# Optimization experiments

Hardware: AMD Instinct MI355X
Metric: run time of the kernel (lower is better)

The kernel has to match this reference:

```python
import jax, jax.numpy as jnp
import numpy as np
from jax import lax

B, DIM, H, W = 16, 256, 64, 64
NH, KD = 8, 16
NH_KD = NH * KD        # 128
DH = 2 * NH_KD         # 256 (attn_ratio=2)
SCALE = KD ** -0.5
PE_LEN = 16


def conv1x1(x, Wt, b):
    # x: [B,Cin,H,W], Wt: [Cout,Cin]
    return jnp.einsum('oi,bihw->bohw', Wt, x) + b[None, :, None, None]


def dwconv3x3(x, Wt, b):
    # depthwise 3x3, pad 1. Wt: [C,1,3,3]
    C = x.shape[1]
    y = lax.conv_general_dilated(x, Wt, window_strides=(1, 1),
                                 padding=((1, 1), (1, 1)),
                                 feature_group_count=C,
                                 dimension_numbers=('NCHW', 'OIHW', 'NCHW'))
    return y + b[None, :, None, None]


def relu6(x):
    return jnp.clip(x, 0.0, 6.0)


def h_sigmoid(x):
    return jnp.clip(x + 3.0, 0.0, 6.0) / 6.0


def interp_linear(pe, N):
    # F.interpolate(mode='linear', align_corners=False). pe: [1,C,S] -> [1,C,N]
    S = pe.shape[-1]
    src = (jnp.arange(N, dtype=jnp.float32) + 0.5) * (S / N) - 0.5
    src = jnp.clip(src, 0.0, S - 1.0)
    lo = jnp.floor(src).astype(jnp.int32)
    hi = jnp.minimum(lo + 1, S - 1)
    w = (src - lo.astype(jnp.float32))[None, None, :]
    return pe[..., lo] * (1.0 - w) + pe[..., hi] * w


def axial_attn(qm, km, vm, pe_q, pe_k, N):
    # qm,km: [B,NH_KD,N] squeezed q/k means; vm: [B,DH,N]
    qn = (qm + interp_linear(pe_q, N)).reshape(B, NH, KD, N).transpose(0, 1, 3, 2)  # [B,h,N,kd]
    kn = (km + interp_linear(pe_k, N)).reshape(B, NH, KD, N)                        # [B,h,kd,N]
    vn = vm.reshape(B, NH, DH // NH, N).transpose(0, 1, 3, 2)                       # [B,h,N,d]
    attn = jax.nn.softmax(jnp.einsum('bhik,bhkj->bhij', qn, kn) * SCALE, axis=-1)
    xx = jnp.einsum('bhij,bhjd->bhid', attn, vn)                                    # [B,h,N,d]
    return xx.transpose(0, 1, 3, 2).reshape(B, DH, N)


def reference(x, Wq, bq, Wk, bk, Wv, bv, W_dw, b_dw, W_pw, b_pw,
              W_row, b_row, W_col, b_col, W_proj, b_proj,
              pe_rowq, pe_rowk, pe_colq, pe_colk):
    q = conv1x1(x, Wq, bq)   # [B,NH_KD,H,W]
    k = conv1x1(x, Wk, bk)   # [B,NH_KD,H,W]
    v = conv1x1(x, Wv, bv)   # [B,DH,H,W]

    qkv = jnp.concatenate([q, k, v], axis=1)        # [B,2*DH,H,W]
    qkv = relu6(dwconv3x3(qkv, W_dw, b_dw))
    qkv = conv1x1(qkv, W_pw, b_pw)                  # [B,DIM,H,W]

    # row attention (squeeze over W)
    xx_row = axial_attn(q.mean(-1), k.mean(-1), v.mean(-1), pe_rowq, pe_rowk, H)
    xx_row = conv1x1(relu6(xx_row[..., None]), W_row, b_row)          # [B,DH,H,1]

    # column attention (squeeze over H)
    xx_col = axial_attn(q.mean(-2), k.mean(-2), v.mean(-2), pe_colq, pe_colk, W)
    xx_col = conv1x1(relu6(xx_col[:, :, None, :]), W_col, b_col)      # [B,DH,1,W]

    xx = v + (xx_row + xx_col)                      # broadcast to [B,DH,H,W]
    xx = conv1x1(relu6(xx), W_proj, b_proj)         # [B,DIM,H,W]
    return h_sigmoid(xx) * qkv


def setup_inputs() -> dict:
    key = jax.random.key(0)
    ks = iter(jax.random.split(key, 32))

    def n(shape, fan_in=None):
        s = 1.0 if fan_in is None else 1.0 / np.sqrt(fan_in)
        return jax.random.normal(next(ks), shape, jnp.float32) * s

    return {
        'x': n((B, DIM, H, W)),
        'Wq': n((NH_KD, DIM), DIM), 'bq': n((NH_KD,), DIM),
        'Wk': n((NH_KD, DIM), DIM), 'bk': n((NH_KD,), DIM),
        'Wv': n((DH, DIM), DIM), 'bv': n((DH,), DIM),
        'W_dw': n((2 * DH, 1, 3, 3), 9), 'b_dw': n((2 * DH,), 9),
        'W_pw': n((DIM, 2 * DH), 2 * DH), 'b_pw': n((DIM,), 2 * DH),
        'W_row': n((DH, DH), DH), 'b_row': n((DH,), DH),
        'W_col': n((DH, DH), DH), 'b_col': n((DH,), DH),
        'W_proj': n((DIM, DH), DH), 'b_proj': n((DIM,), DH),
        'pe_rowq': n((1, NH_KD, PE_LEN)), 'pe_rowk': n((1, NH_KD, PE_LEN)),
        'pe_colq': n((1, NH_KD, PE_LEN)), 'pe_colk': n((1, NH_KD, PE_LEN)),
    }
```

## Files before the change

### kernel.cpp

```cpp
#include <hip/hip_runtime.h>


typedef short s16x8 __attribute__((ext_vector_type(8)));
typedef short s16x4 __attribute__((ext_vector_type(4)));
typedef float f32x4 __attribute__((ext_vector_type(4)));
typedef unsigned short ushort_t;

#define OFF_QKVS 0ULL
#define OFF_DWO  67108864ULL
#define OFF_VMOD 134217728ULL
#define OFF_XBF  167772160ULL
#define OFF_MR   201326592ULL
#define OFF_MC   203423744ULL
#define OFF_XXA  205520896ULL
#define OFF_XRCT 207618048ULL
#define OFF_WQKV 209715200ULL
#define OFF_WPW  209977344ULL
#define OFF_WPR  210239488ULL
#define OFF_BQKV 210370560ULL

__device__ __forceinline__ float bf2f(unsigned short u) {
  unsigned int x = ((unsigned int)u) << 16;
  return __builtin_bit_cast(float, x);
}
__device__ __forceinline__ unsigned short f2bf(float f) {
  unsigned int x = __builtin_bit_cast(unsigned int, f);
  x += 0x7fffu + ((x >> 16) & 1u);
  return (unsigned short)(x >> 16);
}
__device__ __forceinline__ float relu6f(float v) { return fminf(fmaxf(v, 0.f), 6.f); }

__device__ __forceinline__ void mfma16(f32x4& d, s16x8 a, s16x8 b) {
  asm("v_mfma_f32_16x16x32_bf16 %0, %1, %2, %0" : "+v"(d) : "v"(a), "v"(b));
}

__global__ __launch_bounds__(256) void pack_k(
    const float* __restrict__ Wq, const float* __restrict__ Wk, const float* __restrict__ Wv,
    const float* __restrict__ bq, const float* __restrict__ bk, const float* __restrict__ bv,
    const float* __restrict__ Wpw, const float* __restrict__ Wpr,
    unsigned short* __restrict__ wqkv, unsigned short* __restrict__ wpw,
    unsigned short* __restrict__ wpr, float* __restrict__ bqkv)
{
  const int i = blockIdx.x * 256 + threadIdx.x;
  if (i < 131072) {
    const int o = i >> 8, k = i & 255;
    float v = (o < 128) ? Wq[o * 256 + k]
            : (o < 256) ? Wk[(o - 128) * 256 + k]
                        : Wv[(o - 256) * 256 + k];
    wqkv[i] = f2bf(v);
  } else if (i < 262144) {
    const int j = i - 131072;
    wpw[j] = f2bf(Wpw[j]);
  } else if (i < 327680) {
    const int j = i - 262144;
    wpr[j] = f2bf(Wpr[j]);
  } else if (i < 328192) {
    const int o = i - 327680;
    bqkv[o] = (o < 128) ? bq[o] : (o < 256) ? bk[o - 128] : bv[o - 256];
  }
}

__global__ __launch_bounds__(256) void xt_k(const float* __restrict__ x,
                                            unsigned short* __restrict__ xbf)
{
  __shared__ float tile[64][68];
  const int bid = blockIdx.x;
  const int nt = bid & 63, ct = (bid >> 6) & 3, b = bid >> 8;
  const int n0 = nt * 64, c0 = ct * 64;
  const int tid = threadIdx.x;
  #pragma unroll
  for (int p = 0; p < 4; ++p) {
    const int g = tid + p * 256;
    const int row = g >> 4, ch = g & 15;
    const float4 v = *(const float4*)&x[((size_t)b * 256 + c0 + row) * 4096 + n0 + ch * 4];
    *(float4*)&tile[row][ch * 4] = v;
  }
  __syncthreads();
  #pragma unroll
  for (int p = 0; p < 2; ++p) {
    const int g = tid + p * 256;
    const int nr = g >> 3, cc = g & 7;
    s16x8 o;
    #pragma unroll
    for (int q = 0; q < 8; ++q) o[q] = f2bf(tile[cc * 8 + q][nr]);
    *(s16x8*)&xbf[((size_t)b * 4096 + n0 + nr) * 256 + c0 + cc * 8] = o;
  }
}

template <int ROWS>
__device__ __forceinline__ void stage_rows(const unsigned short* __restrict__ src,
                                           int ld, unsigned short (*S)[72], int tid)
{
  #pragma unroll
  for (int p = 0; p < ROWS / 32; ++p) {
    const int g = tid + p * 256;
    const int r = g >> 3, sl = g & 7;
    *(s16x8*)&S[r][sl * 8] = *(const s16x8*)&src[(size_t)r * ld + sl * 8];
  }
}

__device__ __forceinline__ void compute64(const unsigned short (*As)[72],
                                          const unsigned short (*Xs)[72],
                                          f32x4 (*acc)[2], int wm, int wn, int lane)
{
  #pragma unroll
  for (int ks = 0; ks < 64; ks += 32) {
    s16x8 bF[2], aF[8];
    #pragma unroll
    for (int j = 0; j < 2; ++j)
      bF[j] = *(const s16x8*)&Xs[wn * 32 + j * 16 + (lane & 15)][ks + (lane >> 4) * 8];
    #pragma unroll
    for (int i = 0; i < 8; ++i)
      aF[i] = *(const s16x8*)&As[wm * 128 + i * 16 + (lane & 15)][ks + (lane >> 4) * 8];
    #pragma unroll
    for (int i = 0; i < 8; ++i)
      #pragma unroll
      for (int j = 0; j < 2; ++j)
        mfma16(acc[i][j], aF[i], bF[j]);
  }
}

__global__ __launch_bounds__(256, 2) void qkv_k(
    const unsigned short* __restrict__ wqkv, const float* __restrict__ bias,
    const unsigned short* __restrict__ xbf, unsigned short* __restrict__ qkvs)
{
  __shared__ __align__(16) unsigned short As[256][72];
  __shared__ __align__(16) unsigned short Xs[64][72];
  const int tid = threadIdx.x, lane = tid & 63, wave = tid >> 6;
  const int wm = wave >> 1, wn = wave & 1;
  const int bid = blockIdx.x;
  const int nt = bid & 63, mt = (bid >> 6) & 1, b = bid >> 7;
  const int row0 = mt * 256, col0 = nt * 64;

  f32x4 acc[8][2];
  #pragma unroll
  for (int i = 0; i < 8; ++i)
    #pragma unroll
    for (int j = 0; j < 2; ++j) acc[i][j] = (f32x4){0.f, 0.f, 0.f, 0.f};

  for (int k0 = 0; k0 < 256; k0 += 64) {
    stage_rows<256>(wqkv + (size_t)row0 * 256 + k0, 256, As, tid);
    stage_rows<64>(xbf + ((size_t)b * 4096 + col0) * 256 + k0, 256, Xs, tid);
    __syncthreads();
    compute64(As, Xs, acc, wm, wn, lane);
    __syncthreads();
  }

  #pragma unroll
  for (int i = 0; i < 8; ++i) {
    const int o0 = row0 + wm * 128 + i * 16 + ((lane >> 4) << 2);
    const float4 b4 = *(const float4*)&bias[o0];
    #pragma unroll
    for (int j = 0; j < 2; ++j) {
      const int n = col0 + wn * 32 + j * 16 + (lane & 15);
      s16x4 pk;
      pk[0] = f2bf(acc[i][j][0] + b4.x);
      pk[1] = f2bf(acc[i][j][1] + b4.y);
      pk[2] = f2bf(acc[i][j][2] + b4.z);
      pk[3] = f2bf(acc[i][j][3] + b4.w);
      *(s16x4*)&qkvs[((size_t)b * 4096 + n) * 512 + o0] = pk;
    }
  }
}

__global__ __launch_bounds__(256, 2) void fin_k(
    const unsigned short* __restrict__ wpw, const float* __restrict__ bpw,
    const unsigned short* __restrict__ wpr, const float* __restrict__ bpr,
    const unsigned short* __restrict__ dwo, const unsigned short* __restrict__ vmod,
    float* __restrict__ out)
{
  __shared__ __align__(16) unsigned short As[256][72];
  __shared__ __align__(16) unsigned short Xs[64][72];
  const int tid = threadIdx.x, lane = tid & 63, wave = tid >> 6;
  const int wm = wave >> 1, wn = wave & 1;
  const int bid = blockIdx.x;
  const int nt = bid & 63, b = bid >> 6;
  const int col0 = nt * 64;

  f32x4 apw[8][2], apr[8][2];
  #pragma unroll
  for (int i = 0; i < 8; ++i)
    #pragma unroll
    for (int j = 0; j < 2; ++j) {
      apw[i][j] = (f32x4){0.f, 0.f, 0.f, 0.f};
      apr[i][j] = (f32x4){0.f, 0.f, 0.f, 0.f};
    }

  for (int k0 = 0; k0 < 512; k0 += 64) {
    stage_rows<256>(wpw + k0, 512, As, tid);
    stage_rows<64>(dwo + ((size_t)b * 4096 + col0) * 512 + k0, 512, Xs, tid);
    __syncthreads();
    compute64(As, Xs, apw, wm, wn, lane);
    __syncthreads();
  }
  for (int k0 = 0; k0 < 256; k0 += 64) {
    stage_rows<256>(wpr + k0, 256, As, tid);
    stage_rows<64>(vmod + ((size_t)b * 4096 + col0) * 256 + k0, 256, Xs, tid);
    __syncthreads();
    compute64(As, Xs, apr, wm, wn, lane);
    __syncthreads();
  }

  #pragma unroll
  for (int i = 0; i < 8; ++i) {
    const int o0 = wm * 128 + i * 16 + ((lane >> 4) << 2);
    const float4 bw = *(const float4*)&bpw[o0];
    const float4 bp = *(const float4*)&bpr[o0];
    const float bwv[4] = {bw.x, bw.y, bw.z, bw.w};
    const float bpv[4] = {bp.x, bp.y, bp.z, bp.w};
    #pragma unroll
    for (int j = 0; j < 2; ++j) {
      const int n = col0 + wn * 32 + j * 16 + (lane & 15);
      #pragma unroll
      for (int r = 0; r < 4; ++r) {
        const float hs = fminf(fmaxf(apr[i][j][r] + bpv[r] + 3.f, 0.f), 6.f) * (1.f / 6.f);
        out[((size_t)b * 256 + o0 + r) * 4096 + n] = hs * (apw[i][j][r] + bwv[r]);
      }
    }
  }
}

__global__ __launch_bounds__(256) void mean_k(const unsigned short* __restrict__ qkvs,
                                              float* __restrict__ mr, float* __restrict__ mc)
{
  const int bid = blockIdx.x;
  const int axis = bid & 1, pos = (bid >> 1) & 63, b = bid >> 7;
  const int c = threadIdx.x * 2;
  float s0 = 0.f, s1 = 0.f;
  for (int t = 0; t < 64; ++t) {
    const int n = axis ? (t * 64 + pos) : (pos * 64 + t);
    const unsigned u = *(const unsigned*)&qkvs[((size_t)b * 4096 + n) * 512 + c];
    s0 += bf2f((unsigned short)u);
    s1 += bf2f((unsigned short)(u >> 16));
  }
  float* dst = axis ? mc : mr;
  dst[((size_t)b * 512 + c) * 64 + pos] = s0 * (1.f / 64.f);
  dst[((size_t)b * 512 + c + 1) * 64 + pos] = s1 * (1.f / 64.f);
}

__global__ __launch_bounds__(256) void dwm_k(
    const unsigned short* __restrict__ qkvs, const float* __restrict__ Wdw,
    const float* __restrict__ bdw, unsigned short* __restrict__ dwo)
{
  const int bid = blockIdx.x;
  const int h = bid & 63, b = bid >> 6;
  const int tid = threadIdx.x;
  const int c8 = tid & 63, g = tid >> 6;
  const int c0 = c8 * 8;
  float w9[8][9], bs[8];
  #pragma unroll
  for (int q = 0; q < 8; ++q) {
    bs[q] = bdw[c0 + q];
    #pragma unroll
    for (int j = 0; j < 9; ++j) w9[q][j] = Wdw[(c0 + q) * 9 + j];
  }
  const size_t base = (size_t)b * 4096 * 512;
  for (int p = 0; p < 16; ++p) {
    const int w = g + 4 * p;
    float a[8];
    #pragma unroll
    for (int q = 0; q < 8; ++q) a[q] = bs[q];
    #pragma unroll
    for (int dr = 0; dr < 3; ++dr) {
      const int hh = h + dr - 1;
      if ((unsigned)hh >= 64u) continue;
      #pragma unroll
      for (int dc = 0; dc < 3; ++dc) {
        const int ww = w + dc - 1;
        if ((unsigned)ww >= 64u) continue;
        const s16x8 v = *(const s16x8*)&qkvs[base + (size_t)(hh * 64 + ww) * 512 + c0];
        #pragma unroll
        for (int q = 0; q < 8; ++q)
          a[q] += w9[q][dr * 3 + dc] * bf2f((unsigned short)v[q]);
      }
    }
    s16x8 o8;
    #pragma unroll
    for (int q = 0; q < 8; ++q) o8[q] = f2bf(relu6f(a[q]));
    *(s16x8*)&dwo[base + (size_t)(h * 64 + w) * 512 + c0] = o8;
  }
}

__global__ __launch_bounds__(256) void attn_k(
    const float* __restrict__ mr, const float* __restrict__ mc,
    const float* __restrict__ pe_rq, const float* __restrict__ pe_rk,
    const float* __restrict__ pe_cq, const float* __restrict__ pe_ck,
    float* __restrict__ xxa)
{
  __shared__ float qh[16][69], kh[16][69], vh[32][69], P[64][69];
  const int bid = blockIdx.x;
  const int hd = bid & 7, axis = (bid >> 3) & 1, b = bid >> 4;
  const float* m  = axis ? mc : mr;
  const float* pq = axis ? pe_cq : pe_rq;
  const float* pk = axis ? pe_ck : pe_rk;
  const int tid = threadIdx.x;

  #pragma unroll
  for (int p = 0; p < 4; ++p) {
    const int e = tid + p * 256;
    const int kd = e >> 6, i = e & 63;
    float srcp = 0.25f * (float)i - 0.375f;
    srcp = fminf(fmaxf(srcp, 0.f), 15.f);
    const int lo = (int)srcp;
    const int hi = min(lo + 1, 15);
    const float w = srcp - (float)lo;
    const int cq = hd * 16 + kd;
    qh[kd][i] = m[((size_t)b * 512 + cq) * 64 + i]
              + pq[cq * 16 + lo] * (1.f - w) + pq[cq * 16 + hi] * w;
    kh[kd][i] = m[((size_t)b * 512 + 128 + cq) * 64 + i]
              + pk[cq * 16 + lo] * (1.f - w) + pk[cq * 16 + hi] * w;
  }
  #pragma unroll
  for (int p = 0; p < 8; ++p) {
    const int e = tid + p * 256;
    const int d = e >> 6, j = e & 63;
    vh[d][j] = m[((size_t)b * 512 + 256 + hd * 32 + d) * 64 + j];
  }
  __syncthreads();
  {
    const int i = tid >> 2, j0 = (tid & 3) * 16;
    float qr[16];
    #pragma unroll
    for (int kd = 0; kd < 16; ++kd) qr[kd] = qh[kd][i];
    #pragma unroll
    for (int jj = 0; jj < 16; ++jj) {
      float s = 0.f;
      #pragma unroll
      for (int kd = 0; kd < 16; ++kd) s += qr[kd] * kh[kd][j0 + jj];
      P[i][j0 + jj] = s * 0.25f;
    }
  }
  __syncthreads();
  if (tid < 64) {
    float mx = -1e30f;
    for (int j = 0; j < 64; ++j) mx = fmaxf(mx, P[tid][j]);
    float sum = 0.f;
    for (int j = 0; j < 64; ++j) { const float e = __expf(P[tid][j] - mx); P[tid][j] = e; sum += e; }
    const float inv = 1.f / sum;
    for (int j = 0; j < 64; ++j) P[tid][j] *= inv;
  }
  __syncthreads();
  #pragma unroll
  for (int p = 0; p < 8; ++p) {
    const int e = tid + p * 256;
    const int d = e >> 6, i = e & 63;
    float s = 0.f;
    for (int j = 0; j < 64; ++j) s += P[i][j] * vh[d][j];
    xxa[(((size_t)(b * 2 + axis)) * 256 + hd * 32 + d) * 64 + i] = s;
  }
}

__global__ __launch_bounds__(256) void rc_k(
    const float* __restrict__ xxa, const float* __restrict__ Wrow, const float* __restrict__ brow,
    const float* __restrict__ Wcol, const float* __restrict__ bcol, float* __restrict__ xrct)
{
  __shared__ float stf[256][8];
  const int bid = blockIdx.x;
  const int ic = bid & 7, axis = (bid >> 3) & 1, b = bid >> 4;
  const float* W  = axis ? Wcol : Wrow;
  const float* bi = axis ? bcol : brow;
  const int tid = threadIdx.x;
  {
    const float* srcp = xxa + (((size_t)(b * 2 + axis)) * 256 + tid) * 64 + ic * 8;
    #pragma unroll
    for (int q = 0; q < 8; ++q) stf[tid][q] = relu6f(srcp[q]);
  }
  __syncthreads();
  float acc[8] = {0.f, 0.f, 0.f, 0.f, 0.f, 0.f, 0.f, 0.f};
  for (int c = 0; c < 256; ++c) {
    const float w = W[tid * 256 + c];
    const float4 s0 = *(const float4*)&stf[c][0];
    const float4 s1 = *(const float4*)&stf[c][4];
    acc[0] += w * s0.x; acc[1] += w * s0.y; acc[2] += w * s0.z; acc[3] += w * s0.w;
    acc[4] += w * s1.x; acc[5] += w * s1.y; acc[6] += w * s1.z; acc[7] += w * s1.w;
  }
  const float bb = bi[tid];
  #pragma unroll
  for (int q = 0; q < 8; ++q)
    xrct[(((size_t)(b * 2 + axis)) * 64 + ic * 8 + q) * 256 + tid] = acc[q] + bb;
}

__global__ __launch_bounds__(256) void vmod_k(
    const unsigned short* __restrict__ qkvs, const float* __restrict__ xrct,
    unsigned short* __restrict__ vmod)
{
  const int i = blockIdx.x * 256 + threadIdx.x;
  const int c8 = i & 31;
  const int n  = (i >> 5) & 4095;
  const int b  = i >> 17;
  const int c0 = c8 * 8;
  const int h = n >> 6, w = n & 63;
  const s16x8 v = *(const s16x8*)&qkvs[((size_t)b * 4096 + n) * 512 + 256 + c0];
  const float* xr = &xrct[(((size_t)(b * 2 + 0)) * 64 + h) * 256 + c0];
  const float* xc = &xrct[(((size_t)(b * 2 + 1)) * 64 + w) * 256 + c0];
  const float4 r0 = *(const float4*)&xr[0], r1 = *(const float4*)&xr[4];
  const float4 q0 = *(const float4*)&xc[0], q1 = *(const float4*)&xc[4];
  const float rr[8] = {r0.x, r0.y, r0.z, r0.w, r1.x, r1.y, r1.z, r1.w};
  const float cc[8] = {q0.x, q0.y, q0.z, q0.w, q1.x, q1.y, q1.z, q1.w};
  s16x8 o;
  #pragma unroll
  for (int q = 0; q < 8; ++q)
    o[q] = f2bf(relu6f(bf2f((unsigned short)v[q]) + rr[q] + cc[q]));
  *(s16x8*)&vmod[((size_t)b * 4096 + n) * 256 + c0] = o;
}

extern "C" void kernel_launch(void* const* d_in, const int* in_sizes, int n_in,
                              void* d_out, int out_size, void* d_ws, size_t ws_size,
                              hipStream_t stream)
{
  const float* x    = (const float*)d_in[0];
  const float* Wq   = (const float*)d_in[1];
  const float* bq   = (const float*)d_in[2];
  const float* Wk   = (const float*)d_in[3];
  const float* bk   = (const float*)d_in[4];
  const float* Wv   = (const float*)d_in[5];
  const float* bv   = (const float*)d_in[6];
  const float* Wdw  = (const float*)d_in[7];
  const float* bdw  = (const float*)d_in[8];
  const float* Wpw  = (const float*)d_in[9];
  const float* bpw  = (const float*)d_in[10];
  const float* Wrow = (const float*)d_in[11];
  const float* brow = (const float*)d_in[12];
  const float* Wcol = (const float*)d_in[13];
  const float* bcol = (const float*)d_in[14];
  const float* Wpr  = (const float*)d_in[15];
  const float* bpr  = (const float*)d_in[16];
  const float* perq = (const float*)d_in[17];
  const float* perk = (const float*)d_in[18];
  const float* pecq = (const float*)d_in[19];
  const float* peck = (const float*)d_in[20];

  char* ws = (char*)d_ws;
  unsigned short* qkvs = (unsigned short*)(ws + OFF_QKVS);
  unsigned short* dwo  = (unsigned short*)(ws + OFF_DWO);
  unsigned short* vmod = (unsigned short*)(ws + OFF_VMOD);
  unsigned short* xbf  = (unsigned short*)(ws + OFF_XBF);
  float* mr   = (float*)(ws + OFF_MR);
  float* mc   = (float*)(ws + OFF_MC);
  float* xxa  = (float*)(ws + OFF_XXA);
  float* xrct = (float*)(ws + OFF_XRCT);
  unsigned short* wqkv = (unsigned short*)(ws + OFF_WQKV);
  unsigned short* wpw  = (unsigned short*)(ws + OFF_WPW);
  unsigned short* wpr  = (unsigned short*)(ws + OFF_WPR);
  float* bqkv = (float*)(ws + OFF_BQKV);

  pack_k<<<1282, 256, 0, stream>>>(Wq, Wk, Wv, bq, bk, bv, Wpw, Wpr, wqkv, wpw, wpr, bqkv);
  xt_k<<<4096, 256, 0, stream>>>(x, xbf);

  qkv_k<<<2048, 256, 0, stream>>>(wqkv, bqkv, xbf, qkvs);
  mean_k<<<2048, 256, 0, stream>>>(qkvs, mr, mc);
  attn_k<<<256, 256, 0, stream>>>(mr, mc, perq, perk, pecq, peck, xxa);
  rc_k<<<256, 256, 0, stream>>>(xxa, Wrow, brow, Wcol, bcol, xrct);
  vmod_k<<<8192, 256, 0, stream>>>(qkvs, xrct, vmod);
  dwm_k<<<1024, 256, 0, stream>>>(qkvs, Wdw, bdw, dwo);
  fin_k<<<1024, 256, 0, stream>>>(wpw, bpw, wpr, bpr, dwo, vmod, (float*)d_out);
}
```

Baseline: 246.8 us.

## Fuse row means into QKV GEMM, vmod into final GEMM, sliding-window dwconv

Row means are now reduced from the fp32 accumulators inside the QKV GEMM epilogue, so the row half of the separate mean pass goes away and only column means remain in a smaller kernel. The v-modulation (v + row + col, relu6) is computed while staging the final GEMM's B tile, which removes the vmod intermediate write and re-read. The depthwise conv is rewritten so each thread walks 16 consecutive columns with a rolling 3-column register window, cutting redundant global loads. The costs are extra register pressure, fp32 xrct loads inside the GEMM staging, and a slightly different mean computed from unrounded accumulators.

Measured after the change: 231.3 us. 1.07x faster.

```diff
diff --git a/kernel.cpp b/kernel.cpp
--- a/kernel.cpp
+++ b/kernel.cpp
@@ -4,11 +4,9 @@
 typedef short s16x8 __attribute__((ext_vector_type(8)));
 typedef short s16x4 __attribute__((ext_vector_type(4)));
 typedef float f32x4 __attribute__((ext_vector_type(4)));
-typedef unsigned short ushort_t;
 
 #define OFF_QKVS 0ULL
 #define OFF_DWO  67108864ULL
-#define OFF_VMOD 134217728ULL
 #define OFF_XBF  167772160ULL
 #define OFF_MR   201326592ULL
 #define OFF_MC   203423744ULL
@@ -122,10 +120,12 @@
 
 __global__ __launch_bounds__(256, 2) void qkv_k(
     const unsigned short* __restrict__ wqkv, const float* __restrict__ bias,
-    const unsigned short* __restrict__ xbf, unsigned short* __restrict__ qkvs)
+    const unsigned short* __restrict__ xbf, unsigned short* __restrict__ qkvs,
+    float* __restrict__ mr)
 {
   __shared__ __align__(16) unsigned short As[256][72];
   __shared__ __align__(16) unsigned short Xs[64][72];
+  __shared__ float msum[2][256];
   const int tid = threadIdx.x, lane = tid & 63, wave = tid >> 6;
   const int wm = wave >> 1, wn = wave & 1;
   const int bid = blockIdx.x;
@@ -160,14 +160,106 @@
       pk[3] = f2bf(acc[i][j][3] + b4.w);
       *(s16x4*)&qkvs[((size_t)b * 4096 + n) * 512 + o0] = pk;
     }
-  }
+    #pragma unroll
+    for (int r = 0; r < 4; ++r) {
+      float s = acc[i][0][r] + acc[i][1][r];
+      s += __shfl_xor(s, 1);
+      s += __shfl_xor(s, 2);
+      s += __shfl_xor(s, 4);
+      s += __shfl_xor(s, 8);
+      if ((lane & 15) == 0)
+        msum[wn][wm * 128 + i * 16 + ((lane >> 4) << 2) + r] = s;
+    }
+  }
+  __syncthreads();
+  mr[((size_t)b * 512 + row0 + tid) * 64 + nt] =
+      (msum[0][tid] + msum[1][tid]) * (1.f / 64.f) + bias[row0 + tid];
+}
+
+__global__ __launch_bounds__(256) void mc_k(const unsigned short* __restrict__ qkvs,
+                                            float* __restrict__ mc)
+{
+  const int bid = blockIdx.x;
+  const int pos = bid & 63, b = bid >> 6;
+  const int c = threadIdx.x * 2;
+  float s0 = 0.f, s1 = 0.f;
+  for (int t = 0; t < 64; ++t) {
+    const int n = t * 64 + pos;
+    const unsigned u = *(const unsigned*)&qkvs[((size_t)b * 4096 + n) * 512 + c];
+    s0 += bf2f((unsigned short)u);
+    s1 += bf2f((unsigned short)(u >> 16));
+  }
+  mc[((size_t)b * 512 + c) * 64 + pos] = s0 * (1.f / 64.f);
+  mc[((size_t)b * 512 + c + 1) * 64 + pos] = s1 * (1.f / 64.f);
+}
+
+__global__ __launch_bounds__(256, 2) void dwm_k(
+    const unsigned short* __restrict__ qkvs, const float* __restrict__ Wdw,
+    const float* __restrict__ bdw, unsigned short* __restrict__ dwo)
+{
+  const int bid = blockIdx.x;
+  const int h = bid & 63, b = bid >> 6;
+  const int tid = threadIdx.x;
+  const int c0 = (tid & 63) * 8;
+  const int w0 = (tid >> 6) * 16;
+  float w9[8][9], bs[8];
+  #pragma unroll
+  for (int q = 0; q < 8; ++q) {
+    bs[q] = bdw[c0 + q];
+    #pragma unroll
+    for (int j = 0; j < 9; ++j) w9[q][j] = Wdw[(c0 + q) * 9 + j];
+  }
+  const size_t base = (size_t)b * 4096 * 512;
+  const bool hv0 = h > 0, hv2 = h < 63;
+
+  float col[3][3][8];
+#define LOADCOL(WW, S)                                                        \
+  {                                                                           \
+    const int ww_ = (WW);                                                     \
+    const bool wv_ = (unsigned)ww_ < 64u;                                     \
+    _Pragma("unroll")                                                         \
+    for (int dr = 0; dr < 3; ++dr) {                                          \
+      const bool v_ = wv_ && (dr == 0 ? hv0 : (dr == 2 ? hv2 : true));        \
+      if (v_) {                                                               \
+        const s16x8 t_ = *(const s16x8*)&qkvs[base +                          \
+            ((size_t)((h + dr - 1) * 64 + ww_)) * 512 + c0];                  \
+        _Pragma("unroll")                                                     \
+        for (int q = 0; q < 8; ++q) col[S][dr][q] = bf2f((unsigned short)t_[q]); \
+      } else {                                                                \
+        _Pragma("unroll")                                                     \
+        for (int q = 0; q < 8; ++q) col[S][dr][q] = 0.f;                      \
+      }                                                                       \
+    }                                                                         \
+  }
+
+  LOADCOL(w0 - 1, 0)
+  LOADCOL(w0, 1)
+  #pragma unroll
+  for (int t = 0; t < 16; ++t) {
+    const int sm1 = t % 3, s0 = (t + 1) % 3, sp1 = (t + 2) % 3;
+    LOADCOL(w0 + t + 1, sp1)
+    s16x8 o8;
+    #pragma unroll
+    for (int q = 0; q < 8; ++q) {
+      float a = bs[q];
+      #pragma unroll
+      for (int dr = 0; dr < 3; ++dr) {
+        a += w9[q][dr * 3 + 0] * col[sm1][dr][q];
+        a += w9[q][dr * 3 + 1] * col[s0][dr][q];
+        a += w9[q][dr * 3 + 2] * col[sp1][dr][q];
+      }
+      o8[q] = f2bf(relu6f(a));
+    }
+    *(s16x8*)&dwo[base + (size_t)(h * 64 + w0 + t) * 512 + c0] = o8;
+  }
+#undef LOADCOL
 }
 
 __global__ __launch_bounds__(256, 2) void fin_k(
     const unsigned short* __restrict__ wpw, const float* __restrict__ bpw,
     const unsigned short* __restrict__ wpr, const float* __restrict__ bpr,
-    const unsigned short* __restrict__ dwo, const unsigned short* __restrict__ vmod,
-    float* __restrict__ out)
+    const unsigned short* __restrict__ dwo, const unsigned short* __restrict__ qkvs,
+    const float* __restrict__ xrct, float* __restrict__ out)
 {
   __shared__ __align__(16) unsigned short As[256][72];
   __shared__ __align__(16) unsigned short Xs[64][72];
@@ -193,9 +285,28 @@
     compute64(As, Xs, apw, wm, wn, lane);
     __syncthreads();
   }
+  const float* xr = &xrct[(((size_t)b * 2 + 0) * 64 + nt) * 256];
+  const float* xc = &xrct[(((size_t)b * 2 + 1) * 64) * 256];
   for (int k0 = 0; k0 < 256; k0 += 64) {
     stage_rows<256>(wpr + k0, 256, As, tid);
-    stage_rows<64>(vmod + ((size_t)b * 4096 + col0) * 256 + k0, 256, Xs, tid);
+    #pragma unroll
+    for (int p = 0; p < 2; ++p) {
+      const int g = tid + p * 256;
+      const int r = g >> 3, sl = g & 7;
+      const int kk = k0 + sl * 8;
+      const s16x8 v = *(const s16x8*)&qkvs[((size_t)b * 4096 + col0 + r) * 512 + 256 + kk];
+      const float4 a0 = *(const float4*)&xr[kk];
+      const float4 a1 = *(const float4*)&xr[kk + 4];
+      const float4 c0v = *(const float4*)&xc[(size_t)r * 256 + kk];
+      const float4 c1v = *(const float4*)&xc[(size_t)r * 256 + kk + 4];
+      const float ar[8] = {a0.x, a0.y, a0.z, a0.w, a1.x, a1.y, a1.z, a1.w};
+      const float ac[8] = {c0v.x, c0v.y, c0v.z, c0v.w, c1v.x, c1v.y, c1v.z, c1v.w};
+      s16x8 o;
+      #pragma unroll
+      for (int q = 0; q < 8; ++q)
+        o[q] = f2bf(relu6f(bf2f((unsigned short)v[q]) + ar[q] + ac[q]));
+      *(s16x8*)&Xs[r][sl * 8] = o;
+    }
     __syncthreads();
     compute64(As, Xs, apr, wm, wn, lane);
     __syncthreads();
@@ -217,67 +328,6 @@
         out[((size_t)b * 256 + o0 + r) * 4096 + n] = hs * (apw[i][j][r] + bwv[r]);
       }
     }
-  }
-}
-
-__global__ __launch_bounds__(256) void mean_k(const unsigned short* __restrict__ qkvs,
-                                              float* __restrict__ mr, float* __restrict__ mc)
-{
-  const int bid = blockIdx.x;
-  const int axis = bid & 1, pos = (bid >> 1) & 63, b = bid >> 7;
-  const int c = threadIdx.x * 2;
-  float s0 = 0.f, s1 = 0.f;
-  for (int t = 0; t < 64; ++t) {
-    const int n = axis ? (t * 64 + pos) : (pos * 64 + t);
-    const unsigned u = *(const unsigned*)&qkvs[((size_t)b * 4096 + n) * 512 + c];
-    s0 += bf2f((unsigned short)u);
-    s1 += bf2f((unsigned short)(u >> 16));
-  }
-  float* dst = axis ? mc : mr;
-  dst[((size_t)b * 512 + c) * 64 + pos] = s0 * (1.f / 64.f);
-  dst[((size_t)b * 512 + c + 1) * 64 + pos] = s1 * (1.f / 64.f);
-}
-
-__global__ __launch_bounds__(256) void dwm_k(
-    const unsigned short* __restrict__ qkvs, const float* __restrict__ Wdw,
-    const float* __restrict__ bdw, unsigned short* __restrict__ dwo)
-{
-  const int bid = blockIdx.x;
-  const int h = bid & 63, b = bid >> 6;
-  const int tid = threadIdx.x;
-  const int c8 = tid & 63, g = tid >> 6;
-  const int c0 = c8 * 8;
-  float w9[8][9], bs[8];
-  #pragma unroll
-  for (int q = 0; q < 8; ++q) {
-    bs[q] = bdw[c0 + q];
-    #pragma unroll
-    for (int j = 0; j < 9; ++j) w9[q][j] = Wdw[(c0 + q) * 9 + j];
-  }
-  const size_t base = (size_t)b * 4096 * 512;
-  for (int p = 0; p < 16; ++p) {
-    const int w = g + 4 * p;
-    float a[8];
-    #pragma unroll
-    for (int q = 0; q < 8; ++q) a[q] = bs[q];
-    #pragma unroll
-    for (int dr = 0; dr < 3; ++dr) {
-      const int hh = h + dr - 1;
-      if ((unsigned)hh >= 64u) continue;
-      #pragma unroll
-      for (int dc = 0; dc < 3; ++dc) {
-        const int ww = w + dc - 1;
-        if ((unsigned)ww >= 64u) continue;
-        const s16x8 v = *(const s16x8*)&qkvs[base + (size_t)(hh * 64 + ww) * 512 + c0];
-        #pragma unroll
-        for (int q = 0; q < 8; ++q)
-          a[q] += w9[q][dr * 3 + dc] * bf2f((unsigned short)v[q]);
-      }
-    }
-    s16x8 o8;
-    #pragma unroll
-    for (int q = 0; q < 8; ++q) o8[q] = f2bf(relu6f(a[q]));
-    *(s16x8*)&dwo[base + (size_t)(h * 64 + w) * 512 + c0] = o8;
   }
 }
 
@@ -378,30 +428,6 @@
   #pragma unroll
   for (int q = 0; q < 8; ++q)
     xrct[(((size_t)(b * 2 + axis)) * 64 + ic * 8 + q) * 256 + tid] = acc[q] + bb;
-}
-
-__global__ __launch_bounds__(256) void vmod_k(
-    const unsigned short* __restrict__ qkvs, const float* __restrict__ xrct,
-    unsigned short* __restrict__ vmod)
-{
-  const int i = blockIdx.x * 256 + threadIdx.x;
-  const int c8 = i & 31;
-  const int n  = (i >> 5) & 4095;
-  const int b  = i >> 17;
-  const int c0 = c8 * 8;
-  const int h = n >> 6, w = n & 63;
-  const s16x8 v = *(const s16x8*)&qkvs[((size_t)b * 4096 + n) * 512 + 256 + c0];
-  const float* xr = &xrct[(((size_t)(b * 2 + 0)) * 64 + h) * 256 + c0];
-  const float* xc = &xrct[(((size_t)(b * 2 + 1)) * 64 + w) * 256 + c0];
-  const float4 r0 = *(const float4*)&xr[0], r1 = *(const float4*)&xr[4];
-  const float4 q0 = *(const float4*)&xc[0], q1 = *(const float4*)&xc[4];
-  const float rr[8] = {r0.x, r0.y, r0.z, r0.w, r1.x, r1.y, r1.z, r1.w};
-  const float cc[8] = {q0.x, q0.y, q0.z, q0.w, q1.x, q1.y, q1.z, q1.w};
-  s16x8 o;
-  #pragma unroll
-  for (int q = 0; q < 8; ++q)
-    o[q] = f2bf(relu6f(bf2f((unsigned short)v[q]) + rr[q] + cc[q]));
-  *(s16x8*)&vmod[((size_t)b * 4096 + n) * 256 + c0] = o;
 }
 
 extern "C" void kernel_launch(void* const* d_in, const int* in_sizes, int n_in,
@@ -433,7 +459,6 @@
   char* ws = (char*)d_ws;
   unsigned short* qkvs = (unsigned short*)(ws + OFF_QKVS);
   unsigned short* dwo  = (unsigned short*)(ws + OFF_DWO);
-  unsigned short* vmod = (unsigned short*)(ws + OFF_VMOD);
   unsigned short* xbf  = (unsigned short*)(ws + OFF_XBF);
   float* mr   = (float*)(ws + OFF_MR);
   float* mc   = (float*)(ws + OFF_MC);
@@ -447,11 +472,10 @@
   pack_k<<<1282, 256, 0, stream>>>(Wq, Wk, Wv, bq, bk, bv, Wpw, Wpr, wqkv, wpw, wpr, bqkv);
   xt_k<<<4096, 256, 0, stream>>>(x, xbf);
 
-  qkv_k<<<2048, 256, 0, stream>>>(wqkv, bqkv, xbf, qkvs);
-  mean_k<<<2048, 256, 0, stream>>>(qkvs, mr, mc);
+  qkv_k<<<2048, 256, 0, stream>>>(wqkv, bqkv, xbf, qkvs, mr);
+  dwm_k<<<1024, 256, 0, stream>>>(qkvs, Wdw, bdw, dwo);
+  mc_k<<<1024, 256, 0, stream>>>(qkvs, mc);
   attn_k<<<256, 256, 0, stream>>>(mr, mc, perq, perk, pecq, peck, xxa);
   rc_k<<<256, 256, 0, stream>>>(xxa, Wrow, brow, Wcol, bcol, xrct);
-  vmod_k<<<8192, 256, 0, stream>>>(qkvs, xrct, vmod);
-  dwm_k<<<1024, 256, 0, stream>>>(qkvs, Wdw, bdw, dwo);
-  fin_k<<<1024, 256, 0, stream>>>(wpw, bpw, wpr, bpr, dwo, vmod, (float*)d_out);
-}
+  fin_k<<<1024, 256, 0, stream>>>(wpw, bpw, wpr, bpr, dwo, qkvs, xrct, (float*)d_out);
+}
```
